# Kernel optimization log

Measured on AMD Instinct MI355X. Metric: run time of the kernel, lower is better.

## Reference

```python
import jax, jax.numpy as jnp
import numpy as np

EPS = 1e-6

def _phi(x):
    # elu_feature_map: elu(x) + 1 (positive feature map)
    return jax.nn.elu(x) + 1.0

def setup_inputs() -> dict:
    key = jax.random.key(0)
    ks = jax.random.split(key, 6)
    N, L, S, H, E, D = 4, 2048, 2048, 16, 64, 64
    return {
        "queries1": jax.random.normal(ks[0], (N, L, H, E), jnp.float32),
        "keys1": jax.random.normal(ks[1], (N, S, H, E), jnp.float32),
        "values1": jax.random.normal(ks[2], (N, S, H, D), jnp.float32),
        "queries2": jax.random.normal(ks[3], (N, L, H, E), jnp.float32),
        "keys2": jax.random.normal(ks[4], (N, S, H, E), jnp.float32),
        "values2": jax.random.normal(ks[5], (N, S, H, D), jnp.float32),
        "key_lengths1": jnp.ones((N, S), jnp.float32),
        "key_lengths2": jnp.ones((N, S), jnp.float32),
    }

def _linear_cross(Q, K_other, V_other):
    # Q: (N,L,H,E) featurized queries; K_other: (N,S,H,E) featurized+masked keys
    # KV: (N,H,D,E) ; 'nshd,nshm->nhmd'
    KV = jnp.einsum('nshd,nshm->nhmd', K_other, V_other)
    Ksum = K_other.sum(axis=1)                      # (N,H,E)
    Z = 1.0 / (jnp.einsum('nlhd,nhd->nlh', Q, Ksum) + EPS)
    # 'nlhd,nhmd,nlh->nlhm'
    return jnp.einsum('nlhd,nhmd->nlhm', Q, KV) * Z[..., None]

def reference(queries1, keys1, values1, queries2, keys2, values2,
              key_lengths1, key_lengths2):
    Q1 = _phi(queries1)
    K1 = _phi(keys1) * key_lengths1[:, :, None, None]
    Q2 = _phi(queries2)
    K2 = _phi(keys2) * key_lengths2[:, :, None, None]
    V1 = _linear_cross(Q1, K2, values2)  # stream1 queries attend to stream2 keys/values
    V2 = _linear_cross(Q2, K1, values1)  # stream2 queries attend to stream1 keys/values
    return (V1, V2)
```

## Files before the change

kernel.cpp:

```cpp
#include <hip/hip_runtime.h>

#define NB 4
#define LL 2048
#define SS 2048
#define HH 16
#define EE 64
#define DD 64

#define KVTOT (2*NB*HH*4096)
#define WSFLOATS (KVTOT + 2*NB*HH*64)

typedef short short8 __attribute__((ext_vector_type(8)));
typedef float floatx4 __attribute__((ext_vector_type(4)));

__device__ inline float phi(float x) { return x > 0.f ? x + 1.f : __expf(x); }

__device__ inline unsigned int f2bf(float f) {
    unsigned int x = __float_as_uint(f);
    return (x + 0x7FFFu + ((x >> 16) & 1u)) >> 16;
}
__device__ inline void split_pack(float a, float b, unsigned int &hp, unsigned int &lp) {
    const unsigned int ha = f2bf(a), hb = f2bf(b);
    const float ra = a - __uint_as_float(ha << 16);
    const float rb = b - __uint_as_float(hb << 16);
    hp = (ha & 0xFFFFu) | (hb << 16);
    lp = (f2bf(ra) & 0xFFFFu) | (f2bf(rb) << 16);
}

__global__ __launch_bounds__(256) void kv_kernel(
    const float* __restrict__ k1, const float* __restrict__ v1,
    const float* __restrict__ k2, const float* __restrict__ v2,
    const float* __restrict__ kl1, const float* __restrict__ kl2,
    float* __restrict__ ws)
{
    const int b = blockIdx.x;
    const int chunk = b & 7;
    const int h = (b >> 3) & 15;
    const int n = (b >> 7) & 3;
    const int st = (b >> 9) & 1;
    const float* K  = st ? k1 : k2;
    const float* V  = st ? v1 : v2;
    const float* KL = st ? kl1 : kl2;

    __shared__ __align__(16) unsigned short KtH[64][72];
    __shared__ __align__(16) unsigned short KtL[64][72];
    __shared__ __align__(16) unsigned short VtH[64][72];
    __shared__ __align__(16) unsigned short VtL[64][72];

    const int t = threadIdx.x;
    const int lane = t & 63;
    const int w = t >> 6;
    const int d4 = t & 15;
    const int sp = t >> 4;
    const int c = lane & 15;
    const int q = lane >> 4;

    float ksum[4] = {0.f, 0.f, 0.f, 0.f};
    floatx4 acc[4];
#pragma unroll
    for (int i = 0; i < 4; i++) acc[i] = (floatx4){0.f, 0.f, 0.f, 0.f};

    float4 cur[8]; float curl[4];
    {
        const int sbase = chunk * 256;
#pragma unroll
        for (int i = 0; i < 2; ++i) {
            const int sl = 2 * sp + 32 * i;
            const size_t off = ((size_t)((size_t)n * SS + sbase + sl) * HH + h) * EE + 4 * d4;
            cur[4 * i + 0] = *(const float4*)&K[off];
            cur[4 * i + 1] = *(const float4*)&K[off + HH * EE];
            cur[4 * i + 2] = *(const float4*)&V[off];
            cur[4 * i + 3] = *(const float4*)&V[off + HH * EE];
            curl[2 * i + 0] = KL[(size_t)n * SS + sbase + sl];
            curl[2 * i + 1] = KL[(size_t)n * SS + sbase + sl + 1];
        }
    }

    for (int g = 0; g < 4; ++g) {
        float4 nxt[8]; float nxtl[4];
        if (g < 3) {
            const int sbase = chunk * 256 + (g + 1) * 64;
#pragma unroll
            for (int i = 0; i < 2; ++i) {
                const int sl = 2 * sp + 32 * i;
                const size_t off = ((size_t)((size_t)n * SS + sbase + sl) * HH + h) * EE + 4 * d4;
                nxt[4 * i + 0] = *(const float4*)&K[off];
                nxt[4 * i + 1] = *(const float4*)&K[off + HH * EE];
                nxt[4 * i + 2] = *(const float4*)&V[off];
                nxt[4 * i + 3] = *(const float4*)&V[off + HH * EE];
                nxtl[2 * i + 0] = KL[(size_t)n * SS + sbase + sl];
                nxtl[2 * i + 1] = KL[(size_t)n * SS + sbase + sl + 1];
            }
        }
        if (g) __syncthreads();
#pragma unroll
        for (int i = 0; i < 2; ++i) {
            const int sl = 2 * sp + 32 * i;
            const float4 ka = cur[4 * i + 0], kb = cur[4 * i + 1];
            const float4 va = cur[4 * i + 2], vb = cur[4 * i + 3];
            const float l0 = curl[2 * i + 0], l1 = curl[2 * i + 1];
            const float a0 = phi(ka.x) * l0, a1 = phi(ka.y) * l0;
            const float a2 = phi(ka.z) * l0, a3 = phi(ka.w) * l0;
            const float b0 = phi(kb.x) * l1, b1 = phi(kb.y) * l1;
            const float b2 = phi(kb.z) * l1, b3 = phi(kb.w) * l1;
            ksum[0] += a0 + b0; ksum[1] += a1 + b1;
            ksum[2] += a2 + b2; ksum[3] += a3 + b3;
            unsigned int hp, lp;
            split_pack(a0, b0, hp, lp);
            *(unsigned int*)&KtH[4 * d4 + 0][sl] = hp; *(unsigned int*)&KtL[4 * d4 + 0][sl] = lp;
            split_pack(a1, b1, hp, lp);
            *(unsigned int*)&KtH[4 * d4 + 1][sl] = hp; *(unsigned int*)&KtL[4 * d4 + 1][sl] = lp;
            split_pack(a2, b2, hp, lp);
            *(unsigned int*)&KtH[4 * d4 + 2][sl] = hp; *(unsigned int*)&KtL[4 * d4 + 2][sl] = lp;
            split_pack(a3, b3, hp, lp);
            *(unsigned int*)&KtH[4 * d4 + 3][sl] = hp; *(unsigned int*)&KtL[4 * d4 + 3][sl] = lp;
            split_pack(va.x, vb.x, hp, lp);
            *(unsigned int*)&VtH[4 * d4 + 0][sl] = hp; *(unsigned int*)&VtL[4 * d4 + 0][sl] = lp;
            split_pack(va.y, vb.y, hp, lp);
            *(unsigned int*)&VtH[4 * d4 + 1][sl] = hp; *(unsigned int*)&VtL[4 * d4 + 1][sl] = lp;
            split_pack(va.z, vb.z, hp, lp);
            *(unsigned int*)&VtH[4 * d4 + 2][sl] = hp; *(unsigned int*)&VtL[4 * d4 + 2][sl] = lp;
            split_pack(va.w, vb.w, hp, lp);
            *(unsigned int*)&VtH[4 * d4 + 3][sl] = hp; *(unsigned int*)&VtL[4 * d4 + 3][sl] = lp;
        }
        __syncthreads();
#pragma unroll
        for (int ks = 0; ks < 2; ++ks) {
            const short8 aH = *(const short8*)&VtH[16 * w + c][32 * ks + 8 * q];
            const short8 aL = *(const short8*)&VtL[16 * w + c][32 * ks + 8 * q];
#pragma unroll
            for (int dt = 0; dt < 4; ++dt) {
                const short8 bH = *(const short8*)&KtH[16 * dt + c][32 * ks + 8 * q];
                const short8 bL = *(const short8*)&KtL[16 * dt + c][32 * ks + 8 * q];
                acc[dt] = __builtin_amdgcn_mfma_f32_16x16x32_bf16(aH, bH, acc[dt], 0, 0, 0);
                acc[dt] = __builtin_amdgcn_mfma_f32_16x16x32_bf16(aH, bL, acc[dt], 0, 0, 0);
                acc[dt] = __builtin_amdgcn_mfma_f32_16x16x32_bf16(aL, bH, acc[dt], 0, 0, 0);
            }
        }
        if (g < 3) {
#pragma unroll
            for (int i = 0; i < 8; ++i) cur[i] = nxt[i];
#pragma unroll
            for (int i = 0; i < 4; ++i) curl[i] = nxtl[i];
        }
    }

    const size_t kvbase = ((size_t)((st * NB + n) * HH + h)) * 4096;
#pragma unroll
    for (int dt = 0; dt < 4; ++dt)
#pragma unroll
        for (int r = 0; r < 4; ++r)
            atomicAdd(&ws[kvbase + (size_t)(16 * w + 4 * q + r) * 64 + 16 * dt + c],
                      acc[dt][r]);

    float (*scr)[64] = (float(*)[64])VtL;
    __syncthreads();
    scr[sp][4 * d4 + 0] = ksum[0];
    scr[sp][4 * d4 + 1] = ksum[1];
    scr[sp][4 * d4 + 2] = ksum[2];
    scr[sp][4 * d4 + 3] = ksum[3];
    __syncthreads();
    if (t < 64) {
        float s = 0.f;
#pragma unroll
        for (int i = 0; i < 16; ++i) s += scr[i][t];
        atomicAdd(&ws[KVTOT + ((size_t)(st * NB + n) * HH + h) * 64 + t], s);
    }
}

__global__ __launch_bounds__(256) void out_kernel(
    const float* __restrict__ q1, const float* __restrict__ q2,
    const float* __restrict__ ws, float* __restrict__ out)
{
    const int b = blockIdx.x;
    const int lc = b & 7;
    const int h = (b >> 3) & 15;
    const int n = (b >> 7) & 3;
    const int st = (b >> 9) & 1;
    const float* Q = st ? q2 : q1;
    float* O = out + (size_t)st * ((size_t)NB * LL * HH * DD);

    __shared__ __align__(16) unsigned short BtH[64][72];
    __shared__ __align__(16) unsigned short BtL[64][72];
    __shared__ float Ks[64];
    __shared__ float Zl[256];

    const int t = threadIdx.x;
    const int lane = t & 63;
    const int w = t >> 6;
    const int c = lane & 15;
    const int q = lane >> 4;
    const size_t kvbase = ((size_t)((st * NB + n) * HH + h)) * 4096;

    {
        const int m = t >> 2;
        const int dbase = (t & 3) * 16;
#pragma unroll
        for (int i = 0; i < 4; ++i) {
            const int d0 = dbase + 4 * i;
            const float4 kv = *(const float4*)&ws[kvbase + (size_t)m * 64 + d0];
            unsigned int hp, lp;
            split_pack(kv.x, kv.y, hp, lp);
            *(unsigned int*)&BtH[m][d0]     = hp; *(unsigned int*)&BtL[m][d0]     = lp;
            split_pack(kv.z, kv.w, hp, lp);
            *(unsigned int*)&BtH[m][d0 + 2] = hp; *(unsigned int*)&BtL[m][d0 + 2] = lp;
        }
    }
    if (t < 64) Ks[t] = ws[KVTOT + ((size_t)(st * NB + n) * HH + h) * 64 + t];
    __syncthreads();

    const int lbase = lc * 256;

    {
        const float* qr = &Q[((size_t)((size_t)n * LL + lbase + t) * HH + h) * EE];
        float z = 0.f;
#pragma unroll
        for (int d = 0; d < 64; d += 4) {
            const float4 qv = *(const float4*)&qr[d];
            z += phi(qv.x) * Ks[d] + phi(qv.y) * Ks[d + 1]
               + phi(qv.z) * Ks[d + 2] + phi(qv.w) * Ks[d + 3];
        }
        Zl[t] = 1.f / (z + 1e-6f);
    }

    short8 bH[8], bL[8];
#pragma unroll
    for (int mt = 0; mt < 4; ++mt)
#pragma unroll
        for (int ks = 0; ks < 2; ++ks) {
            bH[2 * mt + ks] = *(const short8*)&BtH[16 * mt + c][32 * ks + 8 * q];
            bL[2 * mt + ks] = *(const short8*)&BtL[16 * mt + c][32 * ks + 8 * q];
        }
    __syncthreads();

    floatx4 acc[16];
#pragma unroll
    for (int i = 0; i < 16; ++i) acc[i] = (floatx4){0.f, 0.f, 0.f, 0.f};

#pragma unroll
    for (int lt = 0; lt < 4; ++lt) {
        const int l = lbase + 64 * w + 16 * lt + c;
        const float* qr = &Q[((size_t)((size_t)n * LL + l) * HH + h) * EE];
#pragma unroll
        for (int ks = 0; ks < 2; ++ks) {
            const int d0 = 32 * ks + 8 * q;
            const float4 qa = *(const float4*)&qr[d0];
            const float4 qb = *(const float4*)&qr[d0 + 4];
            const float p[8] = {phi(qa.x), phi(qa.y), phi(qa.z), phi(qa.w),
                                phi(qb.x), phi(qb.y), phi(qb.z), phi(qb.w)};
            short8 aH, aL;
#pragma unroll
            for (int j = 0; j < 8; ++j) {
                const unsigned int hb = f2bf(p[j]);
                aH[j] = (short)hb;
                aL[j] = (short)f2bf(p[j] - __uint_as_float(hb << 16));
            }
#pragma unroll
            for (int mt = 0; mt < 4; ++mt) {
                acc[4 * lt + mt] = __builtin_amdgcn_mfma_f32_16x16x32_bf16(
                    aH, bH[2 * mt + ks], acc[4 * lt + mt], 0, 0, 0);
                acc[4 * lt + mt] = __builtin_amdgcn_mfma_f32_16x16x32_bf16(
                    aH, bL[2 * mt + ks], acc[4 * lt + mt], 0, 0, 0);
                acc[4 * lt + mt] = __builtin_amdgcn_mfma_f32_16x16x32_bf16(
                    aL, bH[2 * mt + ks], acc[4 * lt + mt], 0, 0, 0);
            }
        }
    }

#pragma unroll
    for (int lt = 0; lt < 4; ++lt) {
#pragma unroll
        for (int r = 0; r < 4; ++r) {
            const int ll = 64 * w + 16 * lt + 4 * q + r;
            const float z = Zl[ll];
            const size_t ro = ((size_t)((size_t)n * LL + lbase + ll) * HH + h) * DD;
#pragma unroll
            for (int mt = 0; mt < 4; ++mt)
                O[ro + 16 * mt + c] = acc[4 * lt + mt][r] * z;
        }
    }
}

extern "C" void kernel_launch(void* const* d_in, const int* in_sizes, int n_in,
                              void* d_out, int out_size, void* d_ws, size_t ws_size,
                              hipStream_t stream) {
    const float* q1  = (const float*)d_in[0];
    const float* k1  = (const float*)d_in[1];
    const float* v1  = (const float*)d_in[2];
    const float* q2  = (const float*)d_in[3];
    const float* k2  = (const float*)d_in[4];
    const float* v2  = (const float*)d_in[5];
    const float* kl1 = (const float*)d_in[6];
    const float* kl2 = (const float*)d_in[7];
    float* ws = (float*)d_ws;
    float* out = (float*)d_out;

    hipMemsetAsync(d_ws, 0, (size_t)WSFLOATS * sizeof(float), stream);
    kv_kernel<<<dim3(1024), dim3(256), 0, stream>>>(k1, v1, k2, v2, kl1, kl2, ws);
    out_kernel<<<dim3(1024), dim3(256), 0, stream>>>(q1, q2, ws, out);
}
```

Baseline: 254.7 us.

## Fuse normalizer into MFMA loop, halve rows per block, prefetch Q early

The out kernel now handles 128 rows per block instead of 256 and launches twice as many blocks. The separate pass that re-read Q to compute the normalizer Z is folded into the MFMA loop. There each lane accumulates a partial dot product with Ksum and reduces it with cross-lane shuffles, which removes the second global read of Q, the Zl shared array and one barrier. The first Q tile is loaded before the KV shared-memory staging to hide latency, and B fragments are read from LDS inside the loop rather than held in registers. This costs more LDS reads and re-stages KV for twice as many blocks.

```diff
diff --git a/kernel.cpp b/kernel.cpp
--- a/kernel.cpp
+++ b/kernel.cpp
@@ -168,22 +168,58 @@
     }
 }
 
+static __device__ __forceinline__ float lt_body(
+    const float4 qa0, const float4 qb0, const float4 qa1, const float4 qb1,
+    const float* Ksp,
+    const unsigned short (*BH)[72], const unsigned short (*BL)[72],
+    const int c, const int q, floatx4* acc)
+{
+    float z = 0.f;
+#pragma unroll
+    for (int ks = 0; ks < 2; ++ks) {
+        const float4 qa = ks ? qa1 : qa0;
+        const float4 qb = ks ? qb1 : qb0;
+        const int co = 32 * ks + 8 * q;
+        const float p[8] = {phi(qa.x), phi(qa.y), phi(qa.z), phi(qa.w),
+                            phi(qb.x), phi(qb.y), phi(qb.z), phi(qb.w)};
+        z += p[0] * Ksp[co + 0] + p[1] * Ksp[co + 1]
+           + p[2] * Ksp[co + 2] + p[3] * Ksp[co + 3]
+           + p[4] * Ksp[co + 4] + p[5] * Ksp[co + 5]
+           + p[6] * Ksp[co + 6] + p[7] * Ksp[co + 7];
+        short8 aH, aL;
+#pragma unroll
+        for (int j = 0; j < 8; ++j) {
+            const unsigned int hb = f2bf(p[j]);
+            aH[j] = (short)hb;
+            aL[j] = (short)f2bf(p[j] - __uint_as_float(hb << 16));
+        }
+#pragma unroll
+        for (int mt = 0; mt < 4; ++mt) {
+            const short8 bH = *(const short8*)&BH[16 * mt + c][co];
+            const short8 bL = *(const short8*)&BL[16 * mt + c][co];
+            acc[mt] = __builtin_amdgcn_mfma_f32_16x16x32_bf16(aH, bH, acc[mt], 0, 0, 0);
+            acc[mt] = __builtin_amdgcn_mfma_f32_16x16x32_bf16(aH, bL, acc[mt], 0, 0, 0);
+            acc[mt] = __builtin_amdgcn_mfma_f32_16x16x32_bf16(aL, bH, acc[mt], 0, 0, 0);
+        }
+    }
+    return z;
+}
+
 __global__ __launch_bounds__(256) void out_kernel(
     const float* __restrict__ q1, const float* __restrict__ q2,
     const float* __restrict__ ws, float* __restrict__ out)
 {
     const int b = blockIdx.x;
-    const int lc = b & 7;
-    const int h = (b >> 3) & 15;
-    const int n = (b >> 7) & 3;
-    const int st = (b >> 9) & 1;
+    const int lc = b & 15;
+    const int h = (b >> 4) & 15;
+    const int n = (b >> 8) & 3;
+    const int st = (b >> 10) & 1;
     const float* Q = st ? q2 : q1;
     float* O = out + (size_t)st * ((size_t)NB * LL * HH * DD);
 
     __shared__ __align__(16) unsigned short BtH[64][72];
     __shared__ __align__(16) unsigned short BtL[64][72];
     __shared__ float Ks[64];
-    __shared__ float Zl[256];
 
     const int t = threadIdx.x;
     const int lane = t & 63;
@@ -191,6 +227,14 @@
     const int c = lane & 15;
     const int q = lane >> 4;
     const size_t kvbase = ((size_t)((st * NB + n) * HH + h)) * 4096;
+    const int lbase = lc * 128;
+
+    const float* qr0 = &Q[((size_t)((size_t)n * LL + lbase + 32 * w + c) * HH + h) * EE];
+    const int d0q = 8 * q;
+    const float4 p00 = *(const float4*)&qr0[d0q];
+    const float4 p01 = *(const float4*)&qr0[d0q + 4];
+    const float4 p02 = *(const float4*)&qr0[d0q + 32];
+    const float4 p03 = *(const float4*)&qr0[d0q + 36];
 
     {
         const int m = t >> 2;
@@ -209,74 +253,35 @@
     if (t < 64) Ks[t] = ws[KVTOT + ((size_t)(st * NB + n) * HH + h) * 64 + t];
     __syncthreads();
 
-    const int lbase = lc * 256;
-
-    {
-        const float* qr = &Q[((size_t)((size_t)n * LL + lbase + t) * HH + h) * EE];
-        float z = 0.f;
-#pragma unroll
-        for (int d = 0; d < 64; d += 4) {
-            const float4 qv = *(const float4*)&qr[d];
-            z += phi(qv.x) * Ks[d] + phi(qv.y) * Ks[d + 1]
-               + phi(qv.z) * Ks[d + 2] + phi(qv.w) * Ks[d + 3];
-        }
-        Zl[t] = 1.f / (z + 1e-6f);
-    }
-
-    short8 bH[8], bL[8];
-#pragma unroll
-    for (int mt = 0; mt < 4; ++mt)
-#pragma unroll
-        for (int ks = 0; ks < 2; ++ks) {
-            bH[2 * mt + ks] = *(const short8*)&BtH[16 * mt + c][32 * ks + 8 * q];
-            bL[2 * mt + ks] = *(const short8*)&BtL[16 * mt + c][32 * ks + 8 * q];
-        }
-    __syncthreads();
-
-    floatx4 acc[16];
-#pragma unroll
-    for (int i = 0; i < 16; ++i) acc[i] = (floatx4){0.f, 0.f, 0.f, 0.f};
-
-#pragma unroll
-    for (int lt = 0; lt < 4; ++lt) {
-        const int l = lbase + 64 * w + 16 * lt + c;
-        const float* qr = &Q[((size_t)((size_t)n * LL + l) * HH + h) * EE];
-#pragma unroll
-        for (int ks = 0; ks < 2; ++ks) {
-            const int d0 = 32 * ks + 8 * q;
-            const float4 qa = *(const float4*)&qr[d0];
-            const float4 qb = *(const float4*)&qr[d0 + 4];
-            const float p[8] = {phi(qa.x), phi(qa.y), phi(qa.z), phi(qa.w),
-                                phi(qb.x), phi(qb.y), phi(qb.z), phi(qb.w)};
-            short8 aH, aL;
-#pragma unroll
-            for (int j = 0; j < 8; ++j) {
-                const unsigned int hb = f2bf(p[j]);
-                aH[j] = (short)hb;
-                aL[j] = (short)f2bf(p[j] - __uint_as_float(hb << 16));
-            }
-#pragma unroll
-            for (int mt = 0; mt < 4; ++mt) {
-                acc[4 * lt + mt] = __builtin_amdgcn_mfma_f32_16x16x32_bf16(
-                    aH, bH[2 * mt + ks], acc[4 * lt + mt], 0, 0, 0);
-                acc[4 * lt + mt] = __builtin_amdgcn_mfma_f32_16x16x32_bf16(
-                    aH, bL[2 * mt + ks], acc[4 * lt + mt], 0, 0, 0);
-                acc[4 * lt + mt] = __builtin_amdgcn_mfma_f32_16x16x32_bf16(
-                    aL, bH[2 * mt + ks], acc[4 * lt + mt], 0, 0, 0);
-            }
-        }
-    }
-
-#pragma unroll
-    for (int lt = 0; lt < 4; ++lt) {
+    floatx4 acc[8];
+#pragma unroll
+    for (int i = 0; i < 8; ++i) acc[i] = (floatx4){0.f, 0.f, 0.f, 0.f};
+
+    float z0 = lt_body(p00, p01, p02, p03, Ks, BtH, BtL, c, q, acc);
+
+    const float* qr1 = qr0 + (size_t)16 * HH * EE;
+    const float4 p10 = *(const float4*)&qr1[d0q];
+    const float4 p11 = *(const float4*)&qr1[d0q + 4];
+    const float4 p12 = *(const float4*)&qr1[d0q + 32];
+    const float4 p13 = *(const float4*)&qr1[d0q + 36];
+    float z1 = lt_body(p10, p11, p12, p13, Ks, BtH, BtL, c, q, acc + 4);
+
+    z0 += __shfl_xor(z0, 16); z0 += __shfl_xor(z0, 32);
+    z1 += __shfl_xor(z1, 16); z1 += __shfl_xor(z1, 32);
+    const float zi0 = 1.f / (z0 + 1e-6f);
+    const float zi1 = 1.f / (z1 + 1e-6f);
+
+#pragma unroll
+    for (int lt = 0; lt < 2; ++lt) {
+        const float zi = lt ? zi1 : zi0;
 #pragma unroll
         for (int r = 0; r < 4; ++r) {
-            const int ll = 64 * w + 16 * lt + 4 * q + r;
-            const float z = Zl[ll];
+            const float zz = __shfl(zi, 4 * q + r);
+            const int ll = 32 * w + 16 * lt + 4 * q + r;
             const size_t ro = ((size_t)((size_t)n * LL + lbase + ll) * HH + h) * DD;
 #pragma unroll
             for (int mt = 0; mt < 4; ++mt)
-                O[ro + 16 * mt + c] = acc[4 * lt + mt][r] * z;
+                O[ro + 16 * mt + c] = acc[4 * lt + mt][r] * zz;
         }
     }
 }
@@ -297,5 +302,5 @@
 
     hipMemsetAsync(d_ws, 0, (size_t)WSFLOATS * sizeof(float), stream);
     kv_kernel<<<dim3(1024), dim3(256), 0, stream>>>(k1, v1, k2, v2, kl1, kl2, ws);
-    out_kernel<<<dim3(1024), dim3(256), 0, stream>>>(q1, q2, ws, out);
-}
+    out_kernel<<<dim3(2048), dim3(256), 0, stream>>>(q1, q2, ws, out);
+}
```

Result: faster. 240.8 us (-5.4%).
